# Kernel tuning notes

Measured on AMD Instinct MI355X. Metric: run time of the kernel, lower is better.

Reference implementation:

```python
import jax, jax.numpy as jnp
import numpy as np

B, N, E = 128, 2048, 32768   # events, nodes per history graph, temporal edges per graph
C, TC, H = 4, 4, 2           # channels, time_channels, heads (hardcoded in source)
DH = C // H
L = 2                        # num_layers


def setup_inputs() -> dict:
    key = jax.random.key(0)
    ks = jax.random.split(key, 16)
    return {
        "x": jax.random.normal(ks[0], (B, N, C), jnp.float32),
        "edge_index": jax.random.randint(ks[1], (B, 2, E), 0, N),
        "edge_time": jax.random.uniform(ks[2], (B, E), jnp.float32),
        "timestamp": jax.random.uniform(ks[3], (B,), jnp.float32),
        "src_index": jax.random.randint(ks[4], (B,), 0, N),
        "dst_index": jax.random.randint(ks[5], (B,), 0, N),
        "time_w": jax.random.normal(ks[6], (TC,), jnp.float32),
        "time_b": jax.random.normal(ks[7], (TC,), jnp.float32),
        "Wq": jax.random.normal(ks[8], (L, C, C), jnp.float32) / np.sqrt(C).astype(np.float32),
        "Wk": jax.random.normal(ks[9], (L, C + TC, C), jnp.float32) / np.sqrt(C + TC).astype(np.float32),
        "Wv": jax.random.normal(ks[10], (L, C + TC, C), jnp.float32) / np.sqrt(C + TC).astype(np.float32),
        "Wo": jax.random.normal(ks[11], (L, C, C), jnp.float32) / np.sqrt(C).astype(np.float32),
        "bo": jnp.zeros((L, C), jnp.float32),
        "W_lin": jax.random.normal(ks[12], (2 * C + TC, 2), jnp.float32) / np.sqrt(2 * C + TC).astype(np.float32),
        "b_lin": jnp.zeros((2,), jnp.float32),
    }


def _time_enc(t, w, b):
    # TimeEncoder: cos(t * w + b)  (Bochner-style functional time encoding)
    return jnp.cos(t[..., None] * w + b)


def _encode(x, src, dst, phi, Wq, Wk, Wv, Wo, bo):
    # seg id per edge: (batch, dst node) -> flat segment for segment softmax
    seg = (jnp.arange(B, dtype=dst.dtype)[:, None] * N + dst).reshape(-1)  # [B*E]
    h = x
    for l in range(L):
        h_src = jnp.take_along_axis(h, src[:, :, None], axis=1)            # [B,E,C] gather source feats
        msg = jnp.concatenate([h_src, phi], axis=-1)                       # [B,E,C+TC]
        q = (h @ Wq[l]).reshape(B, N, C)                                   # [B,N,C]
        k = (msg @ Wk[l]).reshape(B, E, H, DH)
        v = (msg @ Wv[l]).reshape(B, E, H, DH)
        q_e = jnp.take_along_axis(q, dst[:, :, None], axis=1).reshape(B, E, H, DH)
        logits = (q_e * k).sum(-1) / np.float32(np.sqrt(DH))               # [B,E,H]
        lf = logits.reshape(B * E, H)
        m = jax.ops.segment_max(lf, seg, num_segments=B * N)               # stable softmax max
        p = jnp.exp(lf - m[seg])
        s = jax.ops.segment_sum(p, seg, num_segments=B * N)
        agg = jax.ops.segment_sum(p[:, :, None] * v.reshape(B * E, H, DH), seg, num_segments=B * N)
        attn = (agg / jnp.where(s == 0, 1.0, s)[:, :, None]).reshape(B, N, C)
        h = jax.nn.relu(h + attn @ Wo[l] + bo[l])                          # residual + out-proj + relu
    return h


def reference(x, edge_index, edge_time, timestamp, src_index, dst_index,
              time_w, time_b, Wq, Wk, Wv, Wo, bo, W_lin, b_lin):
    src, dst = edge_index[:, 0, :], edge_index[:, 1, :]
    dt = timestamp[:, None] - edge_time                                    # [B,E] time deltas vs query time
    phi = _time_enc(dt, time_w, time_b)                                    # [B,E,TC]
    h = _encode(x, src, dst, phi, Wq, Wk, Wv, Wo, bo)                      # [B,N,C]
    bidx = jnp.arange(B)
    src_x = h[bidx, src_index]                                             # [B,C]
    dst_x = h[bidx, dst_index]                                             # [B,C]
    time_x = _time_enc(timestamp, time_w, time_b)                          # [B,TC]
    feats = jnp.concatenate([src_x, dst_x, time_x], axis=-1)               # [B,12]
    return feats @ W_lin + b_lin                                           # [B,2]
```

## Files before the change

kernel.cpp:

```cpp
#include <hip/hip_runtime.h>

namespace {

constexpr int B = 128, N = 2048, E = 32768;
constexpr int LOG2N = 11, LOG2E = 15;
constexpr int QE = E / 4;
constexpr int LOG2QE = 13;

constexpr size_t OFF_H0 = 0;
constexpr size_t OFF_H1 = 4u * 1024 * 1024;
constexpr size_t OFF_S8 = 8u * 1024 * 1024;
constexpr size_t OFF_RP = 40u * 1024 * 1024;

__global__ __launch_bounds__(1024) void sort_kernel(const int* __restrict__ edge_index,
                                                    const float* __restrict__ edge_time,
                                                    const float* __restrict__ timestamp,
                                                    int2* __restrict__ sorted8,
                                                    int* __restrict__ row_ptr) {
  __shared__ int  cnt[N];
  __shared__ int  partial[1024];
  __shared__ int2 rec[QE];
  int blk = blockIdx.x, b = blk >> 2, q = blk & 3, t = threadIdx.x;

  cnt[t] = 0; cnt[t + 1024] = 0;
  __syncthreads();

  const int* src_arr = edge_index + (((size_t)(2 * b)) << LOG2E) + q * QE;
  const int* dst_arr = edge_index + (((size_t)(2 * b + 1)) << LOG2E) + q * QE;
  const float* et    = edge_time + (((size_t)b) << LOG2E) + q * QE;
  float ts = timestamp[b];

  for (int e = t; e < QE; e += 1024) atomicAdd(&cnt[dst_arr[e]], 1);
  __syncthreads();

  int i0 = 2 * t, i1 = 2 * t + 1;
  int l0 = cnt[i0], l1 = cnt[i1];
  int sum = l0 + l1;
  partial[t] = sum;
  __syncthreads();
  for (int d = 1; d < 1024; d <<= 1) {
    int v = (t >= d) ? partial[t - d] : 0;
    __syncthreads();
    partial[t] += v;
    __syncthreads();
  }
  int run = partial[t] - sum;
  int run2 = run + l0;
  int* rp = row_ptr + (size_t)blk * (N + 1);
  rp[i0] = run;
  rp[i1] = run2;
  if (t == 1023) rp[N] = QE;
  cnt[i0] = run;
  cnt[i1] = run2;
  __syncthreads();

  for (int e = t; e < QE; e += 1024) {
    int dst = dst_arr[e];
    int src = src_arr[e];
    float dt = ts - et[e];
    int pos = atomicAdd(&cnt[dst], 1);
    rec[pos] = make_int2(src, __float_as_int(dt));
  }
  __syncthreads();

  const int4* rec4 = (const int4*)rec;
  int4* out4 = (int4*)(sorted8 + (((size_t)blk) << LOG2QE));
#pragma unroll
  for (int i = t; i < QE / 2; i += 1024) out4[i] = rec4[i];
}

__global__ __launch_bounds__(1024) void layer_kernel(const float4* __restrict__ h_in,
                                                     float4* __restrict__ h_out,
                                                     const int* __restrict__ row_ptr,
                                                     const int2* __restrict__ sorted8,
                                                     const float* __restrict__ tw,
                                                     const float* __restrict__ tb,
                                                     const float* __restrict__ Wq,
                                                     const float* __restrict__ Wk,
                                                     const float* __restrict__ Wv,
                                                     const float* __restrict__ Wo,
                                                     const float* __restrict__ bo) {
  __shared__ float4 lh[N];
  int blk = blockIdx.x, b = blk >> 1, half = blk & 1, t = threadIdx.x;

  const float4* hb = h_in + (((size_t)b) << LOG2N);
  lh[t] = hb[t];
  lh[t + 1024] = hb[t + 1024];

  float twf[4], tbf[4], bof[4], wq[16], wof[16], wk[32], wv[32];
#pragma unroll
  for (int j = 0; j < 4; j++) { twf[j] = tw[j]; tbf[j] = tb[j]; bof[j] = bo[j]; }
#pragma unroll
  for (int j = 0; j < 16; j++) { wq[j] = Wq[j]; wof[j] = Wo[j]; }
#pragma unroll
  for (int j = 0; j < 32; j++) { wk[j] = Wk[j]; wv[j] = Wv[j]; }
  __syncthreads();

  int n = half * 1024 + t;
  float4 hn = lh[n];
  float q0 = hn.x * wq[0] + hn.y * wq[4] + hn.z * wq[8]  + hn.w * wq[12];
  float q1 = hn.x * wq[1] + hn.y * wq[5] + hn.z * wq[9]  + hn.w * wq[13];
  float q2 = hn.x * wq[2] + hn.y * wq[6] + hn.z * wq[10] + hn.w * wq[14];
  float q3 = hn.x * wq[3] + hn.y * wq[7] + hn.z * wq[11] + hn.w * wq[15];

  float m0 = -INFINITY, m1 = -INFINITY;
  float s0 = 0.f, s1 = 0.f, a00 = 0.f, a01 = 0.f, a10 = 0.f, a11 = 0.f;
  const float RS2 = 0.70710678118654752f;

#pragma unroll
  for (int q = 0; q < 4; ++q) {
    int qblk = b * 4 + q;
    const int* rp = row_ptr + (size_t)qblk * (N + 1);
    const int2* srt = sorted8 + (((size_t)qblk) << LOG2QE);
    int beg = rp[n], end = rp[n + 1];
    for (int i = beg; i < end; ++i) {
      int2 rc = srt[i];
      float dt = __int_as_float(rc.y);
      float4 hs = lh[rc.x];
      float msg[8];
      msg[0] = hs.x; msg[1] = hs.y; msg[2] = hs.z; msg[3] = hs.w;
#pragma unroll
      for (int j = 0; j < 4; j++) msg[4 + j] = __cosf(dt * twf[j] + tbf[j]);
      float k0 = 0, k1 = 0, k2 = 0, k3 = 0, v0 = 0, v1 = 0, v2 = 0, v3 = 0;
#pragma unroll
      for (int j = 0; j < 8; j++) {
        k0 += msg[j] * wk[j * 4 + 0]; k1 += msg[j] * wk[j * 4 + 1];
        k2 += msg[j] * wk[j * 4 + 2]; k3 += msg[j] * wk[j * 4 + 3];
        v0 += msg[j] * wv[j * 4 + 0]; v1 += msg[j] * wv[j * 4 + 1];
        v2 += msg[j] * wv[j * 4 + 2]; v3 += msg[j] * wv[j * 4 + 3];
      }
      float l0 = (q0 * k0 + q1 * k1) * RS2;
      float l1 = (q2 * k2 + q3 * k3) * RS2;
      float nm0 = fmaxf(m0, l0);
      float sc0 = __expf(m0 - nm0);
      float p0  = __expf(l0 - nm0);
      s0 = s0 * sc0 + p0; a00 = a00 * sc0 + p0 * v0; a01 = a01 * sc0 + p0 * v1; m0 = nm0;
      float nm1 = fmaxf(m1, l1);
      float sc1 = __expf(m1 - nm1);
      float p1  = __expf(l1 - nm1);
      s1 = s1 * sc1 + p1; a10 = a10 * sc1 + p1 * v2; a11 = a11 * sc1 + p1 * v3; m1 = nm1;
    }
  }
  float d0 = (s0 == 0.f) ? 1.f : s0;
  float d1 = (s1 == 0.f) ? 1.f : s1;
  float at0 = a00 / d0, at1 = a01 / d0, at2 = a10 / d1, at3 = a11 / d1;
  float o0 = bof[0] + at0 * wof[0] + at1 * wof[4] + at2 * wof[8]  + at3 * wof[12];
  float o1 = bof[1] + at0 * wof[1] + at1 * wof[5] + at2 * wof[9]  + at3 * wof[13];
  float o2 = bof[2] + at0 * wof[2] + at1 * wof[6] + at2 * wof[10] + at3 * wof[14];
  float o3 = bof[3] + at0 * wof[3] + at1 * wof[7] + at2 * wof[11] + at3 * wof[15];
  h_out[(((size_t)b) << LOG2N) + n] =
      make_float4(fmaxf(hn.x + o0, 0.f), fmaxf(hn.y + o1, 0.f),
                  fmaxf(hn.z + o2, 0.f), fmaxf(hn.w + o3, 0.f));
}

__global__ void final_kernel(const float4* __restrict__ h,
                             const int* __restrict__ src_index, const int* __restrict__ dst_index,
                             const float* __restrict__ timestamp,
                             const float* __restrict__ tw,
                             const float* __restrict__ tb,
                             const float* __restrict__ W_lin,
                             const float* __restrict__ b_lin,
                             float* __restrict__ out) {
  int b = threadIdx.x;
  if (b >= B) return;
  float4 sx = h[(((size_t)b) << LOG2N) + src_index[b]];
  float4 dx = h[(((size_t)b) << LOG2N) + dst_index[b]];
  float ts = timestamp[b];
  float f[12];
  f[0] = sx.x; f[1] = sx.y; f[2] = sx.z; f[3] = sx.w;
  f[4] = dx.x; f[5] = dx.y; f[6] = dx.z; f[7] = dx.w;
#pragma unroll
  for (int j = 0; j < 4; j++) f[8 + j] = __cosf(ts * tw[j] + tb[j]);
#pragma unroll
  for (int c = 0; c < 2; c++) {
    float o = b_lin[c];
#pragma unroll
    for (int j = 0; j < 12; j++) o += f[j] * W_lin[j * 2 + c];
    out[b * 2 + c] = o;
  }
}

}

extern "C" void kernel_launch(void* const* d_in, const int* in_sizes, int n_in,
                              void* d_out, int out_size, void* d_ws, size_t ws_size,
                              hipStream_t stream) {
  (void)in_sizes; (void)n_in; (void)out_size; (void)ws_size;
  const float* x         = (const float*)d_in[0];
  const int*   edge_idx  = (const int*)d_in[1];
  const float* edge_time = (const float*)d_in[2];
  const float* timestamp = (const float*)d_in[3];
  const int*   src_index = (const int*)d_in[4];
  const int*   dst_index = (const int*)d_in[5];
  const float* time_w    = (const float*)d_in[6];
  const float* time_b    = (const float*)d_in[7];
  const float* Wq        = (const float*)d_in[8];
  const float* Wk        = (const float*)d_in[9];
  const float* Wv        = (const float*)d_in[10];
  const float* Wo        = (const float*)d_in[11];
  const float* bo        = (const float*)d_in[12];
  const float* W_lin     = (const float*)d_in[13];
  const float* b_lin     = (const float*)d_in[14];

  char* ws = (char*)d_ws;
  float4* h0      = (float4*)(ws + OFF_H0);
  float4* h1      = (float4*)(ws + OFF_H1);
  int2*   sorted8 = (int2*)(ws + OFF_S8);
  int*    row_ptr = (int*)(ws + OFF_RP);

  sort_kernel<<<4 * B, 1024, 0, stream>>>(edge_idx, edge_time, timestamp, sorted8, row_ptr);

  layer_kernel<<<2 * B, 1024, 0, stream>>>((const float4*)x, h1, row_ptr, sorted8,
                                           time_w, time_b,
                                           Wq + 0 * 16, Wk + 0 * 32, Wv + 0 * 32,
                                           Wo + 0 * 16, bo + 0 * 4);
  layer_kernel<<<2 * B, 1024, 0, stream>>>(h1, h0, row_ptr, sorted8,
                                           time_w, time_b,
                                           Wq + 1 * 16, Wk + 1 * 32, Wv + 1 * 32,
                                           Wo + 1 * 16, bo + 1 * 4);

  final_kernel<<<1, 128, 0, stream>>>(h0, src_index, dst_index, timestamp, time_w, time_b,
                                      W_lin, b_lin, (float*)d_out);
}
```

Baseline: 186.5 us.

## Fold query into key weights, merge edge loops, use shuffle-based scan

The sort kernel's 1024-wide shared-memory Hillis-Steele scan is replaced with a wavefront shuffle scan plus a small cross-wave scan, cutting many block-wide barriers. In the layer kernel, the query vector and the scale factor are folded into the key weights ahead of time, so each edge computes the two attention logits directly instead of the full key vector. The four per-quarter edge loops are flattened into one loop that prefetches the next record, and online softmax now uses a single exp per head. Wo and bo loads move after the loop to lower register pressure. The flattened loop adds stage-switching control flow, and a node with no edges still reads one sorted record.

Result: faster. 168.0 us (-9.9%).

```diff
diff --git a/kernel.cpp b/kernel.cpp
--- a/kernel.cpp
+++ b/kernel.cpp
@@ -18,7 +18,7 @@
                                                     int2* __restrict__ sorted8,
                                                     int* __restrict__ row_ptr) {
   __shared__ int  cnt[N];
-  __shared__ int  partial[1024];
+  __shared__ int  wsum[16];
   __shared__ int2 rec[QE];
   int blk = blockIdx.x, b = blk >> 2, q = blk & 3, t = threadIdx.x;
 
@@ -36,15 +36,27 @@
   int i0 = 2 * t, i1 = 2 * t + 1;
   int l0 = cnt[i0], l1 = cnt[i1];
   int sum = l0 + l1;
-  partial[t] = sum;
-  __syncthreads();
-  for (int d = 1; d < 1024; d <<= 1) {
-    int v = (t >= d) ? partial[t - d] : 0;
-    __syncthreads();
-    partial[t] += v;
-    __syncthreads();
-  }
-  int run = partial[t] - sum;
+  int lane = t & 63, wid = t >> 6;
+  int incl = sum;
+#pragma unroll
+  for (int d = 1; d < 64; d <<= 1) {
+    int v = __shfl_up(incl, d, 64);
+    if (lane >= d) incl += v;
+  }
+  if (lane == 63) wsum[wid] = incl;
+  __syncthreads();
+  if (t < 16) {
+    int v = wsum[t];
+    int inc = v;
+#pragma unroll
+    for (int d = 1; d < 16; d <<= 1) {
+      int u = __shfl_up(inc, d, 16);
+      if (t >= d) inc += u;
+    }
+    wsum[t] = inc - v;
+  }
+  __syncthreads();
+  int run = wsum[wid] + (incl - sum);
   int run2 = run + l0;
   int* rp = row_ptr + (size_t)blk * (N + 1);
   rp[i0] = run;
@@ -87,63 +99,124 @@
   lh[t] = hb[t];
   lh[t + 1024] = hb[t + 1024];
 
-  float twf[4], tbf[4], bof[4], wq[16], wof[16], wk[32], wv[32];
-#pragma unroll
-  for (int j = 0; j < 4; j++) { twf[j] = tw[j]; tbf[j] = tb[j]; bof[j] = bo[j]; }
-#pragma unroll
-  for (int j = 0; j < 16; j++) { wq[j] = Wq[j]; wof[j] = Wo[j]; }
-#pragma unroll
-  for (int j = 0; j < 32; j++) { wk[j] = Wk[j]; wv[j] = Wv[j]; }
+  float twf[4], tbf[4], wq[16], wkh[16], wkp[16], wvh[16], wvp[16];
+#pragma unroll
+  for (int j = 0; j < 4; j++) { twf[j] = tw[j]; tbf[j] = tb[j]; }
+#pragma unroll
+  for (int j = 0; j < 16; j++) wq[j] = Wq[j];
+#pragma unroll
+  for (int j = 0; j < 16; j++) { wkh[j] = Wk[j]; wkp[j] = Wk[16 + j]; }
+#pragma unroll
+  for (int j = 0; j < 16; j++) { wvh[j] = Wv[j]; wvp[j] = Wv[16 + j]; }
   __syncthreads();
 
   int n = half * 1024 + t;
   float4 hn = lh[n];
-  float q0 = hn.x * wq[0] + hn.y * wq[4] + hn.z * wq[8]  + hn.w * wq[12];
-  float q1 = hn.x * wq[1] + hn.y * wq[5] + hn.z * wq[9]  + hn.w * wq[13];
-  float q2 = hn.x * wq[2] + hn.y * wq[6] + hn.z * wq[10] + hn.w * wq[14];
-  float q3 = hn.x * wq[3] + hn.y * wq[7] + hn.z * wq[11] + hn.w * wq[15];
+  const float RS2 = 0.70710678118654752f;
+  float q0 = (hn.x * wq[0] + hn.y * wq[4] + hn.z * wq[8]  + hn.w * wq[12]) * RS2;
+  float q1 = (hn.x * wq[1] + hn.y * wq[5] + hn.z * wq[9]  + hn.w * wq[13]) * RS2;
+  float q2 = (hn.x * wq[2] + hn.y * wq[6] + hn.z * wq[10] + hn.w * wq[14]) * RS2;
+  float q3 = (hn.x * wq[3] + hn.y * wq[7] + hn.z * wq[11] + hn.w * wq[15]) * RS2;
+
+  float wH0[4], wH1[4], wA[4], wB[4];
+#pragma unroll
+  for (int i = 0; i < 4; i++) {
+    wH0[i] = q0 * wkh[i * 4 + 0] + q1 * wkh[i * 4 + 1];
+    wH1[i] = q2 * wkh[i * 4 + 2] + q3 * wkh[i * 4 + 3];
+    wA[i]  = q0 * wkp[i * 4 + 0] + q1 * wkp[i * 4 + 1];
+    wB[i]  = q2 * wkp[i * 4 + 2] + q3 * wkp[i * 4 + 3];
+  }
+
+  int stage = 0;
+  int addr, rem, total;
+  int b1, b2, b3, c1, c2, c3;
+  {
+    const int* rp0 = row_ptr + (size_t)(b * 4 + 0) * (N + 1);
+    const int* rp1 = row_ptr + (size_t)(b * 4 + 1) * (N + 1);
+    const int* rp2 = row_ptr + (size_t)(b * 4 + 2) * (N + 1);
+    const int* rp3 = row_ptr + (size_t)(b * 4 + 3) * (N + 1);
+    int s0 = rp0[n], e0 = rp0[n + 1];
+    int s1 = rp1[n], e1 = rp1[n + 1];
+    int s2 = rp2[n], e2 = rp2[n + 1];
+    int s3 = rp3[n], e3 = rp3[n + 1];
+    int c0 = e0 - s0; c1 = e1 - s1; c2 = e2 - s2; c3 = e3 - s3;
+    total = c0 + c1 + c2 + c3;
+    addr = ((b * 4 + 0) << LOG2QE) + s0; rem = c0;
+    b1 = ((b * 4 + 1) << LOG2QE) + s1;
+    b2 = ((b * 4 + 2) << LOG2QE) + s2;
+    b3 = ((b * 4 + 3) << LOG2QE) + s3;
+  }
+  while (rem == 0 && stage < 3) {
+    ++stage;
+    addr = (stage == 1) ? b1 : (stage == 2) ? b2 : b3;
+    rem  = (stage == 1) ? c1 : (stage == 2) ? c2 : c3;
+  }
 
   float m0 = -INFINITY, m1 = -INFINITY;
-  float s0 = 0.f, s1 = 0.f, a00 = 0.f, a01 = 0.f, a10 = 0.f, a11 = 0.f;
-  const float RS2 = 0.70710678118654752f;
-
-#pragma unroll
-  for (int q = 0; q < 4; ++q) {
-    int qblk = b * 4 + q;
-    const int* rp = row_ptr + (size_t)qblk * (N + 1);
-    const int2* srt = sorted8 + (((size_t)qblk) << LOG2QE);
-    int beg = rp[n], end = rp[n + 1];
-    for (int i = beg; i < end; ++i) {
-      int2 rc = srt[i];
-      float dt = __int_as_float(rc.y);
-      float4 hs = lh[rc.x];
-      float msg[8];
-      msg[0] = hs.x; msg[1] = hs.y; msg[2] = hs.z; msg[3] = hs.w;
-#pragma unroll
-      for (int j = 0; j < 4; j++) msg[4 + j] = __cosf(dt * twf[j] + tbf[j]);
-      float k0 = 0, k1 = 0, k2 = 0, k3 = 0, v0 = 0, v1 = 0, v2 = 0, v3 = 0;
-#pragma unroll
-      for (int j = 0; j < 8; j++) {
-        k0 += msg[j] * wk[j * 4 + 0]; k1 += msg[j] * wk[j * 4 + 1];
-        k2 += msg[j] * wk[j * 4 + 2]; k3 += msg[j] * wk[j * 4 + 3];
-        v0 += msg[j] * wv[j * 4 + 0]; v1 += msg[j] * wv[j * 4 + 1];
-        v2 += msg[j] * wv[j * 4 + 2]; v3 += msg[j] * wv[j * 4 + 3];
-      }
-      float l0 = (q0 * k0 + q1 * k1) * RS2;
-      float l1 = (q2 * k2 + q3 * k3) * RS2;
-      float nm0 = fmaxf(m0, l0);
-      float sc0 = __expf(m0 - nm0);
-      float p0  = __expf(l0 - nm0);
-      s0 = s0 * sc0 + p0; a00 = a00 * sc0 + p0 * v0; a01 = a01 * sc0 + p0 * v1; m0 = nm0;
-      float nm1 = fmaxf(m1, l1);
-      float sc1 = __expf(m1 - nm1);
-      float p1  = __expf(l1 - nm1);
-      s1 = s1 * sc1 + p1; a10 = a10 * sc1 + p1 * v2; a11 = a11 * sc1 + p1 * v3; m1 = nm1;
+  float s0v = 0.f, s1v = 0.f, a00 = 0.f, a01 = 0.f, a10 = 0.f, a11 = 0.f;
+
+  int2 rcCur = sorted8[addr];
+  for (int it = 0; it < total; ++it) {
+    int2 rc = rcCur;
+    ++addr; --rem;
+    while (rem == 0 && stage < 3) {
+      ++stage;
+      addr = (stage == 1) ? b1 : (stage == 2) ? b2 : b3;
+      rem  = (stage == 1) ? c1 : (stage == 2) ? c2 : c3;
     }
-  }
-  float d0 = (s0 == 0.f) ? 1.f : s0;
-  float d1 = (s1 == 0.f) ? 1.f : s1;
-  float at0 = a00 / d0, at1 = a01 / d0, at2 = a10 / d1, at3 = a11 / d1;
+    rcCur = sorted8[addr];
+
+    float dt = __int_as_float(rc.y);
+    float4 hs = lh[rc.x];
+    float ph0 = __cosf(dt * twf[0] + tbf[0]);
+    float ph1 = __cosf(dt * twf[1] + tbf[1]);
+    float ph2 = __cosf(dt * twf[2] + tbf[2]);
+    float ph3 = __cosf(dt * twf[3] + tbf[3]);
+
+    float l0 = hs.x * wH0[0] + hs.y * wH0[1] + hs.z * wH0[2] + hs.w * wH0[3]
+             + ph0 * wA[0] + ph1 * wA[1] + ph2 * wA[2] + ph3 * wA[3];
+    float l1 = hs.x * wH1[0] + hs.y * wH1[1] + hs.z * wH1[2] + hs.w * wH1[3]
+             + ph0 * wB[0] + ph1 * wB[1] + ph2 * wB[2] + ph3 * wB[3];
+
+    float v0 = hs.x * wvh[0] + hs.y * wvh[4] + hs.z * wvh[8]  + hs.w * wvh[12]
+             + ph0 * wvp[0] + ph1 * wvp[4] + ph2 * wvp[8]  + ph3 * wvp[12];
+    float v1 = hs.x * wvh[1] + hs.y * wvh[5] + hs.z * wvh[9]  + hs.w * wvh[13]
+             + ph0 * wvp[1] + ph1 * wvp[5] + ph2 * wvp[9]  + ph3 * wvp[13];
+    float v2 = hs.x * wvh[2] + hs.y * wvh[6] + hs.z * wvh[10] + hs.w * wvh[14]
+             + ph0 * wvp[2] + ph1 * wvp[6] + ph2 * wvp[10] + ph3 * wvp[14];
+    float v3 = hs.x * wvh[3] + hs.y * wvh[7] + hs.z * wvh[11] + hs.w * wvh[15]
+             + ph0 * wvp[3] + ph1 * wvp[7] + ph2 * wvp[11] + ph3 * wvp[15];
+
+    float d0 = l0 - m0;
+    float e0 = __expf(fminf(d0, -d0));
+    bool  g0 = d0 > 0.f;
+    float p0  = g0 ? 1.f : e0;
+    float sc0 = g0 ? e0 : 1.f;
+    m0 = fmaxf(m0, l0);
+    s0v = s0v * sc0 + p0;
+    a00 = a00 * sc0 + p0 * v0;
+    a01 = a01 * sc0 + p0 * v1;
+    float d1 = l1 - m1;
+    float e1 = __expf(fminf(d1, -d1));
+    bool  g1 = d1 > 0.f;
+    float p1  = g1 ? 1.f : e1;
+    float sc1 = g1 ? e1 : 1.f;
+    m1 = fmaxf(m1, l1);
+    s1v = s1v * sc1 + p1;
+    a10 = a10 * sc1 + p1 * v2;
+    a11 = a11 * sc1 + p1 * v3;
+  }
+
+  float den0 = (s0v == 0.f) ? 1.f : s0v;
+  float den1 = (s1v == 0.f) ? 1.f : s1v;
+  float at0 = a00 / den0, at1 = a01 / den0, at2 = a10 / den1, at3 = a11 / den1;
+
+  float wof[16], bof[4];
+#pragma unroll
+  for (int j = 0; j < 16; j++) wof[j] = Wo[j];
+#pragma unroll
+  for (int j = 0; j < 4; j++) bof[j] = bo[j];
+
   float o0 = bof[0] + at0 * wof[0] + at1 * wof[4] + at2 * wof[8]  + at3 * wof[12];
   float o1 = bof[1] + at0 * wof[1] + at1 * wof[5] + at2 * wof[9]  + at3 * wof[13];
   float o2 = bof[2] + at0 * wof[2] + at1 * wof[6] + at2 * wof[10] + at3 * wof[14];
```
